# Kernel tuning notes

Measured on AMD Instinct MI355X. Metric: run time of the kernel, lower is better.

Reference implementation:

```python
import jax, jax.numpy as jnp
import numpy as np

A = -0.75  # torch bicubic coefficient
SCALES = [1.0, 0.9, 0.8, 0.7, 0.6]  # level=5
SOFTMAX_SCALE = 10.0
RES_SCALE = 1.0
ESCAPE_NAN = 1e-4


def _cubic_w(d):
    d = jnp.abs(d)
    return jnp.where(d <= 1.0, ((A + 2.0) * d - (A + 3.0)) * d * d + 1.0,
                     jnp.where(d < 2.0, ((A * d - 5.0 * A) * d + 8.0 * A) * d - 4.0 * A, 0.0))


def _resize_axis(x, out_size, axis):
    # bicubic, align_corners=True, 4-tap cubic conv with border clamp (matches torch)
    in_size = x.shape[axis]
    src = jnp.arange(out_size, dtype=jnp.float32) * (float(in_size - 1) / float(out_size - 1))
    i0 = jnp.floor(src).astype(jnp.int32)
    frac = src - i0.astype(jnp.float32)
    idx = jnp.clip(jnp.stack([i0 - 1, i0, i0 + 1, i0 + 2], 0), 0, in_size - 1)  # [4,out]
    w = jnp.stack([_cubic_w(frac + 1.0), _cubic_w(frac), _cubic_w(1.0 - frac), _cubic_w(2.0 - frac)], 0)  # [4,out]
    xm = jnp.moveaxis(x, axis, 0)
    g = xm[idx]  # [4,out,...]
    out = jnp.einsum('ko...,ko->o...', g, w)
    return jnp.moveaxis(out, 0, axis)


def bicubic_resize(x, oh, ow):
    return _resize_axis(_resize_axis(x, oh, 2), ow, 3)


def prelu(x, a):
    return jnp.where(x >= 0, x, a * x)


def conv1x1(x, W, b):
    # x [B,C,H,W], W [O,C], b [O]
    return jnp.einsum('oc,bchw->bohw', W, x) + b[None, :, None, None]


def extract_patches(x):
    # x [B,C,H,W] -> [B, H*W, C, 3, 3], 'same' padding, stride 1 (torch unfold order C,kh,kw)
    B, C, H, Wd = x.shape
    xp = jnp.pad(x, ((0, 0), (0, 0), (1, 1), (1, 1)))
    sl = [xp[:, :, dy:dy + H, dx:dx + Wd] for dy in range(3) for dx in range(3)]
    p = jnp.stack(sl, 0).reshape(3, 3, B, C, H, Wd)
    p = jnp.transpose(p, (2, 4, 5, 3, 0, 1))  # [B,H,W,C,3,3]
    return p.reshape(B, H * Wd, C, 3, 3)


def setup_inputs() -> dict:
    key = jax.random.key(0)
    ks = jax.random.split(key, 8)
    B, C, H, Wd = 2, 64, 64, 64
    Cm = 32
    return {
        'input': jax.random.normal(ks[0], (B, C, H, Wd), jnp.float32),
        'input_ref': jax.random.normal(ks[1], (B, C, H, Wd), jnp.float32),
        'Wb': jax.random.normal(ks[2], (Cm, C), jnp.float32) * 0.1,
        'bb': jax.random.normal(ks[3], (Cm,), jnp.float32) * 0.01,
        'Wm': jax.random.normal(ks[4], (Cm, C), jnp.float32) * 0.1,
        'bm': jax.random.normal(ks[5], (Cm,), jnp.float32) * 0.01,
        'Wa': jax.random.normal(ks[6], (C, C), jnp.float32) * 0.1,
        'ba': jax.random.normal(ks[7], (C,), jnp.float32) * 0.01,
        'a_prelu': jnp.full((1,), 0.25, jnp.float32),
    }


def reference(input, input_ref, Wb, bb, Wm, bm, Wa, ba, a_prelu):
    B, C, H, Wd = input.shape
    a = a_prelu[0]
    match_base = prelu(conv1x1(input, Wb, bb), a)  # [B,Cm,H,W]

    w_list, rw_list = [], []
    for s in SCALES:
        ref = input_ref if s == 1.0 else bicubic_resize(input_ref, int(H * s), int(Wd * s))
        base = prelu(conv1x1(ref, Wa, ba), a)   # conv_assembly
        rw_list.append(extract_patches(base))   # [B,Li,C,3,3]
        m = prelu(conv1x1(ref, Wm, bm), a)      # conv_match
        w_list.append(extract_patches(m))       # [B,Li,Cm,3,3]
    w = jnp.concatenate(w_list, axis=1)    # [B,L,Cm,3,3]
    rw = jnp.concatenate(rw_list, axis=1)  # [B,L,C,3,3]

    dn = ('NCHW', 'OIHW', 'NCHW')

    def per_sample(xi, wi, rwi):
        # xi [Cm,H,W]; wi [L,Cm,3,3]; rwi [L,C,3,3]
        nrm = jnp.maximum(jnp.sqrt(jnp.sum(wi * wi, axis=(1, 2, 3), keepdims=True)), ESCAPE_NAN)
        wn = wi / nrm
        scores = jax.lax.conv_general_dilated(xi[None], wn, (1, 1), [(1, 1), (1, 1)], dimension_numbers=dn)[0]  # [L,H,W]
        yi = jax.nn.softmax(scores * SOFTMAX_SCALE, axis=0)
        # conv_transpose2d(yi, rwi, stride=1, padding=1) == conv2d with flipped, transposed kernel, pad 1
        k = jnp.transpose(rwi, (1, 0, 2, 3))[:, :, ::-1, ::-1]  # [C,L,3,3]
        out = jax.lax.conv_general_dilated(yi[None], k, (1, 1), [(1, 1), (1, 1)], dimension_numbers=dn)[0] / 4.0
        return out  # [C,H,W]

    y = jax.vmap(per_sample)(match_base, w, rw)
    return y + input * RES_SCALE
```

## Files before the change

### kernel.cpp

```cpp
#include <hip/hip_runtime.h>
#include <stdint.h>


typedef __attribute__((ext_vector_type(8))) short bf16x8;
typedef __attribute__((ext_vector_type(4))) float f32x4;
typedef unsigned short ushort_t;

#define L_TOT  13326
#define NCHT   417
#define NPIX   4096
#define BCHUNK_E 9216
#define RCHUNK_E 18432
#define LOG2E10 14.4269504f
#define CT 256

__device__ __forceinline__ float cubw(float d) {
  d = fabsf(d);
  if (d <= 1.f) return (1.25f * d - 2.25f) * d * d + 1.f;
  if (d < 2.f)  return ((-0.75f * d + 3.75f) * d - 6.f) * d + 3.f;
  return 0.f;
}

__device__ __forceinline__ void decode_l(int l, int& S, int& off) {
  if (l < 4096)       { S = 64; off = 0; }
  else if (l < 7345)  { S = 57; off = 4096; }
  else if (l < 9946)  { S = 51; off = 7345; }
  else if (l < 11882) { S = 44; off = 9946; }
  else                { S = 38; off = 11882; }
}

__device__ __forceinline__ ushort_t f2bf(float f) {
  union { float f; uint32_t u; } v; v.f = f;
  uint32_t r = (v.u + 0x7fffu + ((v.u >> 16) & 1u)) >> 16;
  return (ushort_t)r;
}

__device__ __forceinline__ float preluf(float x, float a) { return x >= 0.f ? x : a * x; }

__device__ __forceinline__ void gll16(const ushort_t* g, ushort_t* l) {
  __builtin_amdgcn_global_load_lds(
      (const __attribute__((address_space(1))) unsigned int*)g,
      (__attribute__((address_space(3))) unsigned int*)l, 16, 0, 0);
}

__global__ void k_convref(const float* __restrict__ inref,
                          const float* __restrict__ Wm, const float* __restrict__ bm,
                          const float* __restrict__ Wa, const float* __restrict__ ba,
                          const float* __restrict__ ap,
                          float* __restrict__ mref, float* __restrict__ aref) {
  __shared__ float T[64][CT];
  __shared__ float Wy[CT][5], Wx[CT][5];
  __shared__ int   IY[CT], IX[CT];
  int blk = blockIdx.x;
  int oh = blk & 1; int lt = (blk >> 1) % 53; int b = blk / 106;
  int l0 = lt * CT;
  int tid = threadIdx.x;
  float a = ap[0];
  {
    int gl = l0 + tid;
    if (gl < L_TOT) {
      int S, off; decode_l(gl, S, off);
      int li = gl - off; int ly = li / S, lx = li % S;
      if (S == 64) {
        IY[tid] = -1; IX[tid] = ly * 64 + lx;
      } else {
        float sc = (float)(63.0 / (double)(S - 1));
        float sy = (float)ly * sc, sx = (float)lx * sc;
        int iy = (int)floorf(sy), ix = (int)floorf(sx);
        float fy = sy - (float)iy, fx = sx - (float)ix;
        IY[tid] = iy; IX[tid] = ix;
        Wy[tid][0] = cubw(fy + 1.f); Wy[tid][1] = cubw(fy);
        Wy[tid][2] = cubw(1.f - fy); Wy[tid][3] = cubw(2.f - fy);
        Wx[tid][0] = cubw(fx + 1.f); Wx[tid][1] = cubw(fx);
        Wx[tid][2] = cubw(1.f - fx); Wx[tid][3] = cubw(2.f - fx);
      }
    }
  }
  __syncthreads();
  for (int i = tid; i < 64 * CT; i += 256) {
    int c = i >> 8; int l2 = i & 255;
    int gl = l0 + l2;
    float val = 0.f;
    if (gl < L_TOT) {
      const float* img = inref + (size_t)(b * 64 + c) * 4096;
      int iy = IY[l2];
      if (iy == -1) {
        val = img[IX[l2]];
      } else {
        int ix = IX[l2];
        #pragma unroll
        for (int t = 0; t < 4; ++t) {
          int ty = iy - 1 + t; ty = ty < 0 ? 0 : (ty > 63 ? 63 : ty);
          float rv = 0.f;
          #pragma unroll
          for (int u = 0; u < 4; ++u) {
            int tx = ix - 1 + u; tx = tx < 0 ? 0 : (tx > 63 ? 63 : tx);
            rv += Wx[l2][u] * img[ty * 64 + tx];
          }
          val += Wy[l2][t] * rv;
        }
      }
    }
    T[c][l2] = val;
  }
  __syncthreads();
  int gl = l0 + tid;
  if (gl >= L_TOT) return;
  for (int oc = oh * 48; oc < oh * 48 + 48; ++oc) {
    const float* Wrow; float s;
    if (oc < 32) { Wrow = Wm + oc * 64; s = bm[oc]; }
    else         { Wrow = Wa + (oc - 32) * 64; s = ba[oc - 32]; }
    #pragma unroll 8
    for (int c = 0; c < 64; ++c) s += Wrow[c] * T[c][tid];
    s = preluf(s, a);
    if (oc < 32) mref[(size_t)(b * 32 + oc) * L_TOT + gl] = s;
    else         aref[(size_t)(b * 64 + oc - 32) * L_TOT + gl] = s;
  }
}

__global__ void k_mb(const float* __restrict__ input, const float* __restrict__ Wb,
                     const float* __restrict__ bb, const float* __restrict__ ap,
                     float* __restrict__ mbb, int n) {
  int idx = blockIdx.x * 256 + threadIdx.x;
  if (idx >= n) return;
  int p = idx % NPIX; int cm = (idx / NPIX) % 32; int b = idx / (32 * NPIX);
  float a = ap[0];
  float acc = bb[cm];
  for (int c = 0; c < 64; ++c) acc += Wb[cm * 64 + c] * input[(size_t)(b * 64 + c) * NPIX + p];
  mbb[(size_t)(b * 32 + cm) * NPIX + p] = preluf(acc, a);
}

__global__ void k_stage1(const float* __restrict__ mref, const float* __restrict__ mbb,
                         float* __restrict__ ssq, float* __restrict__ ssqA, int n) {
  int idx = blockIdx.x * 256 + threadIdx.x;
  if (idx >= n) return;
  if (idx < 2 * L_TOT) {
    int l = idx % L_TOT; int b = idx / L_TOT;
    float s = 0.f;
    for (int c = 0; c < 32; ++c) { float v = mref[(size_t)(b * 32 + c) * L_TOT + l]; s += v * v; }
    ssq[idx] = s;
  } else {
    int j = idx - 2 * L_TOT;
    int p = j % NPIX; int b = j / NPIX;
    float s = 0.f;
    for (int c = 0; c < 32; ++c) { float v = mbb[(size_t)(b * 32 + c) * NPIX + p]; s += v * v; }
    ssqA[j] = s;
  }
}

__global__ void k_stage2(const float* __restrict__ ssq, const float* __restrict__ ssqA,
                         float* __restrict__ invn, float* __restrict__ Mlog, int n) {
  int idx = blockIdx.x * 256 + threadIdx.x;
  if (idx >= n) return;
  if (idx < 2 * L_TOT) {
    int l = idx % L_TOT; int b = idx / L_TOT;
    int S, off; decode_l(l, S, off);
    int li = l - off; int ly = li / S, lx = li % S;
    float acc = 0.f;
    for (int dy = -1; dy <= 1; ++dy) {
      int ny = ly + dy; if (ny < 0 || ny >= S) continue;
      for (int dx = -1; dx <= 1; ++dx) {
        int nx = lx + dx; if (nx < 0 || nx >= S) continue;
        acc += ssq[(size_t)b * L_TOT + off + ny * S + nx];
      }
    }
    float nrm = sqrtf(acc); nrm = fmaxf(nrm, 1e-4f);
    invn[idx] = 1.f / nrm;
  } else {
    int j = idx - 2 * L_TOT;
    int p = j % NPIX; int b = j / NPIX;
    int y = p / 64, x = p % 64;
    float acc = 0.f;
    for (int dy = -1; dy <= 1; ++dy) {
      int ny = y + dy; if (ny < 0 || ny >= 64) continue;
      for (int dx = -1; dx <= 1; ++dx) {
        int nx = x + dx; if (nx < 0 || nx >= 64) continue;
        acc += ssqA[(size_t)b * NPIX + ny * 64 + nx];
      }
    }
    float qn = sqrtf(acc);
    float m = fmaxf(0.7f * qn, qn - 7.f);
    Mlog[j] = LOG2E10 * m;
  }
}

#define N_BS (2 * NCHT * 1152)
#define N_AIM (2 * NPIX * 36)
#define N_RS (2 * NCHT * 576 * 4)
__global__ void k_pack(const float* __restrict__ mref, const float* __restrict__ invn,
                       const float* __restrict__ mbb, const float* __restrict__ aref,
                       ushort_t* __restrict__ Bs, ushort_t* __restrict__ Am,
                       ushort_t* __restrict__ Rs, int n) {
  int idx = blockIdx.x * 256 + threadIdx.x;
  if (idx >= n) return;
  ushort_t v[8];
  if (idx < N_BS) {
    int segp = idx % 36; int col = (idx / 36) % 32;
    int ch = (idx / 1152) % NCHT; int b = idx / (1152 * NCHT);
    int segl = (segp & ~3) | ((segp & 3) ^ ((col >> 1) & 3));
    int l = ch * 32 + col;
    if (l < L_TOT) {
      int S, off; decode_l(l, S, off);
      int li = l - off; int ly = li / S, lx = li % S;
      float iv = invn[(size_t)b * L_TOT + l];
      #pragma unroll
      for (int e = 0; e < 8; ++e) {
        int k = segl * 8 + e;
        int c = k / 9; int r = k % 9; int dy = r / 3 - 1, dx = r % 3 - 1;
        int ny = ly + dy, nx = lx + dx;
        float val = 0.f;
        if (ny >= 0 && ny < S && nx >= 0 && nx < S)
          val = mref[(size_t)(b * 32 + c) * L_TOT + off + ny * S + nx] * iv;
        v[e] = f2bf(val);
      }
    } else {
      #pragma unroll
      for (int e = 0; e < 8; ++e) v[e] = 0;
    }
    *(uint4*)(Bs + ((size_t)(b * NCHT + ch) * BCHUNK_E + col * 288 + segp * 8)) = *(const uint4*)v;
  } else if (idx < N_BS + N_AIM) {
    int j = idx - N_BS;
    int k8 = j % 36; int p = (j / 36) % NPIX; int b = j / (36 * NPIX);
    int y = p / 64, x = p % 64;
    #pragma unroll
    for (int e = 0; e < 8; ++e) {
      int k = k8 * 8 + e;
      int c = k / 9; int r = k % 9; int dy = r / 3 - 1, dx = r % 3 - 1;
      int ny = y + dy, nx = x + dx;
      float val = 0.f;
      if (ny >= 0 && ny < 64 && nx >= 0 && nx < 64)
        val = mbb[(size_t)(b * 32 + c) * NPIX + ny * 64 + nx];
      v[e] = f2bf(val);
    }
    *(uint4*)(Am + ((size_t)(b * NPIX + p) * 288 + k8 * 8)) = *(const uint4*)v;
  } else {
    int j = idx - N_BS - N_AIM;
    int phys = j & 3; int q = j >> 2;
    int col = q % 576; q /= 576;
    int ch = q % NCHT; int b = q / NCHT;
    int c = col / 9; int r = col % 9; int dy = r / 3 - 1, dx = r % 3 - 1;
    int seg = phys ^ ((col >> 1) & 3);
    int lbase = ch * 32 + seg * 8;
    #pragma unroll
    for (int e = 0; e < 8; ++e) {
      int l = lbase + e;
      float val = 0.f;
      if (l < L_TOT) {
        int S, off; decode_l(l, S, off);
        int li = l - off; int ly = li / S, lx = li % S;
        int ny = ly + dy, nx = lx + dx;
        if (ny >= 0 && ny < S && nx >= 0 && nx < S)
          val = aref[(size_t)(b * 64 + c) * L_TOT + off + ny * S + nx];
      }
      v[e] = f2bf(val);
    }
    *(uint4*)(Rs + ((size_t)(b * NCHT + ch) * RCHUNK_E + col * 32 + phys * 8)) = *(const uint4*)v;
  }
}

__global__ __launch_bounds__(512, 2) void k_attn64(const ushort_t* __restrict__ Am,
                                                   const ushort_t* __restrict__ Bs,
                                                   const ushort_t* __restrict__ Rs,
                                                   const float* __restrict__ Mlog,
                                                   float* __restrict__ Og,
                                                   float* __restrict__ Ol) {
  __shared__ ushort_t Rl[3][RCHUNK_E];
  __shared__ ushort_t Bl[2][BCHUNK_E];
  __shared__ ushort_t Pl[2][2048];
  int tid = threadIdx.x;
  int xcd = blockIdx.x & 7; int slot = blockIdx.x >> 3;
  int group = xcd >> 1;
  int spl = group & 1; int b = group >> 1;
  int tile = slot * 2 + (xcd & 1);
  int p0 = tile * 64;
  int wave = tid >> 6, lane = tid & 63, quad = lane >> 4, ln = lane & 15;
  int rbS = wave & 3, cbh = wave >> 2;
  int g = wave & 3, zrh = wave >> 2;
  int c0 = spl ? 209 : 0, c1 = spl ? NCHT : 209;

  bf16x8 af[9];
  {
    const ushort_t* arow = Am + (size_t)(b * NPIX + p0 + rbS * 16 + ln) * 288;
    #pragma unroll
    for (int kk = 0; kk < 9; ++kk) af[kk] = *(const bf16x8*)(arow + kk * 32 + quad * 8);
  }
  float mlg[4];
  #pragma unroll
  for (int r = 0; r < 4; ++r)
    mlg[r] = Mlog[(size_t)b * NPIX + p0 + rbS * 16 + quad * 4 + r];

  f32x4 acc[2][9];
  #pragma unroll
  for (int h = 0; h < 2; ++h)
    #pragma unroll
    for (int t = 0; t < 9; ++t) { acc[h][t][0] = acc[h][t][1] = acc[h][t][2] = acc[h][t][3] = 0.f; }
  float psum[4] = {0.f, 0.f, 0.f, 0.f};

  const ushort_t* RsB = Rs + (size_t)b * NCHT * RCHUNK_E + lane * 8;
  const ushort_t* BsB = Bs + (size_t)b * NCHT * BCHUNK_E + lane * 8;

  {
    const ushort_t* sB0 = BsB + (size_t)c0 * BCHUNK_E;
    ushort_t* dB0 = Bl[c0 & 1];
    #pragma unroll
    for (int u = wave; u < 18; u += 8) gll16(sB0 + u * 512, dB0 + u * 512);
    const ushort_t* sB1 = BsB + (size_t)(c0 + 1) * BCHUNK_E;
    ushort_t* dB1 = Bl[(c0 + 1) & 1];
    #pragma unroll
    for (int u = wave; u < 18; u += 8) gll16(sB1 + u * 512, dB1 + u * 512);
    const ushort_t* sR = RsB + (size_t)c0 * RCHUNK_E;
    ushort_t* dR = Rl[c0 % 3];
    #pragma unroll
    for (int u = wave; u < 36; u += 8) gll16(sR + u * 512, dR + u * 512);
  }
  __syncthreads();

  int col32 = cbh * 16 + ln;
  int bswz = (col32 >> 1) & 3;
  int rpar = c0 % 3;
  for (int ch = c0; ch < c1; ++ch) {
    int par = ch & 1;
    int rnext = rpar == 2 ? 0 : rpar + 1;
    f32x4 sa, sb;
    sa[0] = sa[1] = sa[2] = sa[3] = 0.f;
    sb[0] = sb[1] = sb[2] = sb[3] = 0.f;
    #pragma unroll
    for (int kk = 0; kk < 9; ++kk) {
      int segp = kk * 4 + (quad ^ bswz);
      bf16x8 bf = *(const bf16x8*)&Bl[par][col32 * 288 + segp * 8];
      if (kk == 4 || kk == 5 || kk == 6 || kk == 7)
        sb = __builtin_amdgcn_mfma_f32_16x16x32_bf16(af[kk], bf, sb, 0, 0, 0);
      else
        sa = __builtin_amdgcn_mfma_f32_16x16x32_bf16(af[kk], bf, sa, 0, 0, 0);
    }
    int colw = ch * 32 + col32;
    bool valid = colw < L_TOT;
    #pragma unroll
    for (int r = 0; r < 4; ++r) {
      float sv = sa[r] + sb[r];
      float pv = valid ? exp2f(fmaf(sv, LOG2E10, -mlg[r])) : 0.f;
      int row = rbS * 16 + quad * 4 + r;
      int seg = cbh * 2 + (ln >> 3);
      int swz = seg ^ ((row >> 1) & 3);
      Pl[par][row * 32 + swz * 8 + (ln & 7)] = f2bf(pv);
      psum[r] += pv;
    }
    __syncthreads();
    if (ch + 2 < c1) {
      const ushort_t* sB = BsB + (size_t)(ch + 2) * BCHUNK_E;
      ushort_t* dB = Bl[par];
      #pragma unroll
      for (int u = wave; u < 18; u += 8) gll16(sB + u * 512, dB + u * 512);
    }
    if (ch + 1 < c1) {
      const ushort_t* sR = RsB + (size_t)(ch + 1) * RCHUNK_E;
      ushort_t* dR = Rl[rnext];
      #pragma unroll
      for (int u = wave; u < 36; u += 8) gll16(sR + u * 512, dR + u * 512);
    }
    bf16x8 pf0, pf1;
    {
      int sw = quad ^ ((ln >> 1) & 3);
      pf0 = *(const bf16x8*)&Pl[par][(zrh * 32 + ln) * 32 + sw * 8];
      pf1 = *(const bf16x8*)&Pl[par][(zrh * 32 + 16 + ln) * 32 + sw * 8];
    }
    #pragma unroll
    for (int t = 0; t < 9; ++t) {
      int col = g * 144 + t * 16 + ln;
      int swz = quad ^ ((col >> 1) & 3);
      bf16x8 rf = *(const bf16x8*)&Rl[rpar][col * 32 + swz * 8];
      acc[0][t] = __builtin_amdgcn_mfma_f32_16x16x32_bf16(pf0, rf, acc[0][t], 0, 0, 0);
      acc[1][t] = __builtin_amdgcn_mfma_f32_16x16x32_bf16(pf1, rf, acc[1][t], 0, 0, 0);
    }
    rpar = rnext;
  }

  #pragma unroll
  for (int m = 1; m <= 8; m <<= 1)
    #pragma unroll
    for (int r = 0; r < 4; ++r) psum[r] += __shfl_xor(psum[r], m);
  int sb2 = spl * 2 + b;
  if (ln == 0) {
    #pragma unroll
    for (int r = 0; r < 4; ++r) {
      int row = p0 + rbS * 16 + quad * 4 + r;
      Ol[(size_t)(sb2 * 2 + cbh) * NPIX + row] = psum[r];
    }
  }
  #pragma unroll
  for (int h = 0; h < 2; ++h)
    #pragma unroll
    for (int t = 0; t < 9; ++t) {
      int colg = g * 144 + t * 16 + ln;
      #pragma unroll
      for (int r = 0; r < 4; ++r) {
        int row = p0 + zrh * 32 + h * 16 + quad * 4 + r;
        Og[((size_t)sb2 * NPIX + row) * 576 + colg] = acc[h][t][r];
      }
    }
}

__global__ __launch_bounds__(512, 2) void k_attn128(const ushort_t* __restrict__ Am,
                                                    const ushort_t* __restrict__ Bs,
                                                    const ushort_t* __restrict__ Rs,
                                                    const float* __restrict__ Mlog,
                                                    float* __restrict__ Og,
                                                    float* __restrict__ Ol) {
  __shared__ ushort_t Rl[2][RCHUNK_E];
  __shared__ ushort_t Bl[2][BCHUNK_E];
  __shared__ ushort_t Pl[2][4096];
  int tid = threadIdx.x;
  int xcd = blockIdx.x & 7; int slot = blockIdx.x >> 3;
  int spl = xcd >> 1; int b = xcd & 1;
  int p0 = slot * 128;
  int wave = tid >> 6, lane = tid & 63, quad = lane >> 4, ln = lane & 15;
  int rb = wave;
  int g = wave & 3, zrh = wave >> 2;
  int c0 = (spl * NCHT) >> 2;
  int c1 = ((spl + 1) * NCHT) >> 2;

  bf16x8 af[9];
  {
    const ushort_t* arow = Am + (size_t)(b * NPIX + p0 + rb * 16 + ln) * 288;
    #pragma unroll
    for (int kk = 0; kk < 9; ++kk) af[kk] = *(const bf16x8*)(arow + kk * 32 + quad * 8);
  }
  float mlg[4], psum[4];
  #pragma unroll
  for (int r = 0; r < 4; ++r) {
    mlg[r] = Mlog[(size_t)b * NPIX + p0 + rb * 16 + quad * 4 + r];
    psum[r] = 0.f;
  }
  f32x4 acc[4][9];
  #pragma unroll
  for (int j = 0; j < 4; ++j)
    #pragma unroll
    for (int t = 0; t < 9; ++t) { acc[j][t][0] = acc[j][t][1] = acc[j][t][2] = acc[j][t][3] = 0.f; }

  const ushort_t* RsB = Rs + (size_t)b * NCHT * RCHUNK_E + lane * 8;
  const ushort_t* BsB = Bs + (size_t)b * NCHT * BCHUNK_E + lane * 8;

  auto stageB = [&](int chunk, int sl) {
    const ushort_t* s = BsB + (size_t)chunk * BCHUNK_E;
    ushort_t* d = Bl[sl];
    #pragma unroll
    for (int u = wave; u < 18; u += 8) gll16(s + u * 512, d + u * 512);
  };
  auto stageR = [&](int chunk, int sl) {
    const ushort_t* s = RsB + (size_t)chunk * RCHUNK_E;
    ushort_t* d = Rl[sl];
    #pragma unroll
    for (int u = wave; u < 36; u += 8) gll16(s + u * 512, d + u * 512);
  };

  int bswz = (ln >> 1) & 3;
  int psw = quad ^ ((ln >> 1) & 3);

  stageB(c0, 0);
  stageB(c0 + 1, 1);
  stageR(c0, 0);
  __syncthreads();

  for (int ch = c0; ch < c1; ++ch) {
    int par = ch & 1;
    f32x4 sA0, sB0, sA1, sB1;
    sA0[0]=sA0[1]=sA0[2]=sA0[3]=0.f; sB0[0]=sB0[1]=sB0[2]=sB0[3]=0.f;
    sA1[0]=sA1[1]=sA1[2]=sA1[3]=0.f; sB1[0]=sB1[1]=sB1[2]=sB1[3]=0.f;
    #pragma unroll
    for (int kk = 0; kk < 9; ++kk) {
      int segp = kk * 4 + (quad ^ bswz);
      bf16x8 bf0 = *(const bf16x8*)&Bl[par][(ln) * 288 + segp * 8];
      bf16x8 bf1 = *(const bf16x8*)&Bl[par][(16 + ln) * 288 + segp * 8];
      if (kk >= 4 && kk <= 7) {
        sB0 = __builtin_amdgcn_mfma_f32_16x16x32_bf16(af[kk], bf0, sB0, 0, 0, 0);
        sB1 = __builtin_amdgcn_mfma_f32_16x16x32_bf16(af[kk], bf1, sB1, 0, 0, 0);
      } else {
        sA0 = __builtin_amdgcn_mfma_f32_16x16x32_bf16(af[kk], bf0, sA0, 0, 0, 0);
        sA1 = __builtin_amdgcn_mfma_f32_16x16x32_bf16(af[kk], bf1, sA1, 0, 0, 0);
      }
    }
    bool valid0 = ch * 32 + ln < L_TOT;
    bool valid1 = ch * 32 + 16 + ln < L_TOT;
    #pragma unroll
    for (int r = 0; r < 4; ++r) {
      int row = rb * 16 + quad * 4 + r;
      int rsw = (row >> 1) & 3;
      float sv0 = sA0[r] + sB0[r];
      float pv0 = valid0 ? exp2f(fmaf(sv0, LOG2E10, -mlg[r])) : 0.f;
      int seg0 = 0 * 2 + (ln >> 3);
      Pl[par][row * 32 + (seg0 ^ rsw) * 8 + (ln & 7)] = f2bf(pv0);
      float sv1 = sA1[r] + sB1[r];
      float pv1 = valid1 ? exp2f(fmaf(sv1, LOG2E10, -mlg[r])) : 0.f;
      int seg1 = 1 * 2 + (ln >> 3);
      Pl[par][row * 32 + (seg1 ^ rsw) * 8 + (ln & 7)] = f2bf(pv1);
      psum[r] += pv0 + pv1;
    }
    __syncthreads();
    if (ch + 2 < c1) stageB(ch + 2, par);
    if (ch + 1 < c1) stageR(ch + 1, par ^ 1);
    bf16x8 pf[4];
    #pragma unroll
    for (int j = 0; j < 4; ++j)
      pf[j] = *(const bf16x8*)&Pl[par][(zrh * 64 + j * 16 + ln) * 32 + psw * 8];
    #pragma unroll
    for (int t = 0; t < 9; ++t) {
      int col = g * 144 + t * 16 + ln;
      int swz = quad ^ ((col >> 1) & 3);
      bf16x8 rf = *(const bf16x8*)&Rl[par][col * 32 + swz * 8];
      #pragma unroll
      for (int j = 0; j < 4; ++j)
        acc[j][t] = __builtin_amdgcn_mfma_f32_16x16x32_bf16(pf[j], rf, acc[j][t], 0, 0, 0);
    }
  }

  #pragma unroll
  for (int m = 1; m <= 8; m <<= 1)
    #pragma unroll
    for (int r = 0; r < 4; ++r) psum[r] += __shfl_xor(psum[r], m);
  int sb2 = spl * 2 + b;
  if (ln == 0) {
    #pragma unroll
    for (int r = 0; r < 4; ++r) {
      int row = p0 + rb * 16 + quad * 4 + r;
      Ol[(size_t)sb2 * NPIX + row] = psum[r];
    }
  }
  #pragma unroll
  for (int j = 0; j < 4; ++j)
    #pragma unroll
    for (int t = 0; t < 9; ++t) {
      int colg = g * 144 + t * 16 + ln;
      #pragma unroll
      for (int r = 0; r < 4; ++r) {
        int row = p0 + zrh * 64 + j * 16 + quad * 4 + r;
        Og[((size_t)sb2 * NPIX + row) * 576 + colg] = acc[j][t][r];
      }
    }
}

template <int IS128>
__global__ void k_inv(const float* __restrict__ Ol, float* __restrict__ inv, int n) {
  int idx = blockIdx.x * 256 + threadIdx.x;
  if (idx >= n) return;
  int b = idx / NPIX; int p = idx % NPIX;
  float s = 0.f;
  if (IS128) {
    #pragma unroll
    for (int spl = 0; spl < 4; ++spl)
      s += Ol[(size_t)(spl * 2 + b) * NPIX + p];
  } else {
    #pragma unroll
    for (int spl = 0; spl < 2; ++spl)
      #pragma unroll
      for (int cbh = 0; cbh < 2; ++cbh)
        s += Ol[(size_t)(((spl * 2 + b) * 2) + cbh) * NPIX + p];
  }
  inv[idx] = 1.f / s;
}

template <int NSL>
__global__ __launch_bounds__(256) void k_final(const float* __restrict__ Og,
                                               const float* __restrict__ inv,
                                               const float* __restrict__ input,
                                               float* __restrict__ out) {
  __shared__ float Srow[34][577];
  int blk = blockIdx.x;
  int xh = blk & 1; int y = (blk >> 1) & 63; int b = blk >> 7;
  int tid = threadIdx.x;
  const size_t S1 = (size_t)2 * NPIX * 576;
  int x32 = tid & 31, c0 = (tid >> 5) * 8;
  int qx0 = xh * 32 - 1;
  float acc[8];
  #pragma unroll
  for (int i = 0; i < 8; ++i) acc[i] = 0.f;

  for (int j = 0; j < 3; ++j) {
    int qy = y + 1 - j;
    if (qy < 0 || qy >= 64) continue;
    for (int u = tid; u < 34 * 144; u += 256) {
      int k = u / 144; int f4 = u - k * 144;
      int qx = qx0 + k;
      float vx = 0.f, vy = 0.f, vz = 0.f, vw = 0.f;
      if (qx >= 0 && qx < 64) {
        int p = qy * 64 + qx;
        size_t e = ((size_t)b * NPIX + p) * 576 + f4 * 4;
        float iv = inv[b * NPIX + p];
        #pragma unroll
        for (int s = 0; s < NSL; ++s) {
          const float4 t4 = *(const float4*)(Og + e + (size_t)s * S1);
          vx += t4.x; vy += t4.y; vz += t4.z; vw += t4.w;
        }
        vx *= iv; vy *= iv; vz *= iv; vw *= iv;
      }
      float* d = &Srow[k][f4 * 4];
      d[0] = vx; d[1] = vy; d[2] = vz; d[3] = vw;
    }
    __syncthreads();
    #pragma unroll
    for (int i2 = 0; i2 < 3; ++i2) {
      int k = x32 + 2 - i2;
      #pragma unroll
      for (int cc = 0; cc < 8; ++cc)
        acc[cc] += Srow[k][(c0 + cc) * 9 + j * 3 + i2];
    }
    __syncthreads();
  }

  int x = xh * 32 + x32;
  #pragma unroll
  for (int cc = 0; cc < 8; ++cc) {
    int c = c0 + cc;
    int o = ((b * 64 + c) * 64 + y) * 64 + x;
    out[o] = 0.25f * acc[cc] + input[o];
  }
}

extern "C" void kernel_launch(void* const* d_in, const int* in_sizes, int n_in,
                              void* d_out, int out_size, void* d_ws, size_t ws_size,
                              hipStream_t stream) {
  (void)in_sizes; (void)n_in; (void)out_size;
  const float* input = (const float*)d_in[0];
  const float* inref = (const float*)d_in[1];
  const float* Wb = (const float*)d_in[2];
  const float* bb = (const float*)d_in[3];
  const float* Wm = (const float*)d_in[4];
  const float* bm = (const float*)d_in[5];
  const float* Wa = (const float*)d_in[6];
  const float* ba = (const float*)d_in[7];
  const float* ap = (const float*)d_in[8];
  float* out = (float*)d_out;

  char* ws = (char*)d_ws;
  size_t off = 0;
  auto alloc = [&](size_t bytes) -> char* {
    char* p = ws + off; off = (off + bytes + 255) & ~(size_t)255; return p;
  };
  ushort_t* Am   = (ushort_t*)alloc((size_t)2 * NPIX * 288 * 2);
  ushort_t* Bs   = (ushort_t*)alloc((size_t)2 * NCHT * BCHUNK_E * 2);
  ushort_t* Rs   = (ushort_t*)alloc((size_t)2 * NCHT * RCHUNK_E * 2);
  float*    Ol   = (float*)alloc((size_t)16 * NPIX * 4);
  float*    inv  = (float*)alloc((size_t)2 * NPIX * 4);
  float*    Mlog = (float*)alloc((size_t)2 * NPIX * 4);
  float*    ssqA = (float*)alloc((size_t)2 * NPIX * 4);
  size_t og64  = (size_t)4 * NPIX * 576 * 4;
  size_t og128 = og64 * 2;
  bool use128 = (off + og128 + 512) <= ws_size;
  char* big = alloc(use128 ? og128 : og64);
  float* Og = (float*)big;
  size_t eoff = 0;
  auto ealloc = [&](size_t bytes) -> char* {
    char* p = big + eoff; eoff = (eoff + bytes + 255) & ~(size_t)255; return p;
  };
  float* mref = (float*)ealloc((size_t)2 * 32 * L_TOT * 4);
  float* aref = (float*)ealloc((size_t)2 * 64 * L_TOT * 4);
  float* mbb  = (float*)ealloc((size_t)2 * 32 * NPIX * 4);
  float* ssq  = (float*)ealloc((size_t)2 * L_TOT * 4);
  float* invn = (float*)ealloc((size_t)2 * L_TOT * 4);

  k_convref<<<212, 256, 0, stream>>>(inref, Wm, bm, Wa, ba, ap, mref, aref);
  int n3 = 2 * 32 * NPIX;
  k_mb<<<(n3 + 255) / 256, 256, 0, stream>>>(input, Wb, bb, ap, mbb, n3);
  int ns = 2 * L_TOT + 2 * NPIX;
  k_stage1<<<(ns + 255) / 256, 256, 0, stream>>>(mref, mbb, ssq, ssqA, ns);
  k_stage2<<<(ns + 255) / 256, 256, 0, stream>>>(ssq, ssqA, invn, Mlog, ns);
  int np = N_BS + N_AIM + N_RS;
  k_pack<<<(np + 255) / 256, 256, 0, stream>>>(mref, invn, mbb, aref, Bs, Am, Rs, np);

  if (use128) {
    k_attn128<<<256, 512, 0, stream>>>(Am, Bs, Rs, Mlog, Og, Ol);
    k_inv<1><<<(2 * NPIX + 255) / 256, 256, 0, stream>>>(Ol, inv, 2 * NPIX);
    k_final<4><<<256, 256, 0, stream>>>(Og, inv, input, out);
  } else {
    k_attn64<<<256, 512, 0, stream>>>(Am, Bs, Rs, Mlog, Og, Ol);
    k_inv<0><<<(2 * NPIX + 255) / 256, 256, 0, stream>>>(Ol, inv, 2 * NPIX);
    k_final<2><<<256, 256, 0, stream>>>(Og, inv, input, out);
  }
}
```

Measured before the change: 439.0 us.

## Stage pack inputs in LDS, pre-reduce split outputs, split conv accumulators

The pack kernel is rebuilt as one block per chunk or pixel tile. Each block stages the needed window of mref, aref, invn or mbb in shared memory and then builds the Bs, Rs and Am bf16 tiles, so repeated uncached global gathers become LDS reads. On the 128 path, a new k_redog kernel adds the four split partial outputs together so k_final reads a single slice. The 1x1 conv loops in k_convref and k_mb now use four independent accumulators to shorten the dependency chain. The cost is extra launches, a large shared-memory footprint per pack block, and a small change in floating-point summation order.

New measurement: 479.6 us. 9.2% more time.

```diff
diff --git a/kernel.cpp b/kernel.cpp
--- a/kernel.cpp
+++ b/kernel.cpp
@@ -13,6 +13,8 @@
 #define RCHUNK_E 18432
 #define LOG2E10 14.4269504f
 #define CT 256
+#define PKW 169
+#define PKWA 393
 
 __device__ __forceinline__ float cubw(float d) {
   d = fabsf(d);
@@ -107,11 +109,18 @@
   int gl = l0 + tid;
   if (gl >= L_TOT) return;
   for (int oc = oh * 48; oc < oh * 48 + 48; ++oc) {
-    const float* Wrow; float s;
-    if (oc < 32) { Wrow = Wm + oc * 64; s = bm[oc]; }
-    else         { Wrow = Wa + (oc - 32) * 64; s = ba[oc - 32]; }
-    #pragma unroll 8
-    for (int c = 0; c < 64; ++c) s += Wrow[c] * T[c][tid];
+    const float* Wrow; float bias;
+    if (oc < 32) { Wrow = Wm + oc * 64; bias = bm[oc]; }
+    else         { Wrow = Wa + (oc - 32) * 64; bias = ba[oc - 32]; }
+    float s0 = 0.f, s1 = 0.f, s2 = 0.f, s3 = 0.f;
+    #pragma unroll 4
+    for (int c = 0; c < 64; c += 4) {
+      s0 += Wrow[c]     * T[c][tid];
+      s1 += Wrow[c + 1] * T[c + 1][tid];
+      s2 += Wrow[c + 2] * T[c + 2][tid];
+      s3 += Wrow[c + 3] * T[c + 3][tid];
+    }
+    float s = bias + ((s0 + s1) + (s2 + s3));
     s = preluf(s, a);
     if (oc < 32) mref[(size_t)(b * 32 + oc) * L_TOT + gl] = s;
     else         aref[(size_t)(b * 64 + oc - 32) * L_TOT + gl] = s;
@@ -125,8 +134,16 @@
   if (idx >= n) return;
   int p = idx % NPIX; int cm = (idx / NPIX) % 32; int b = idx / (32 * NPIX);
   float a = ap[0];
-  float acc = bb[cm];
-  for (int c = 0; c < 64; ++c) acc += Wb[cm * 64 + c] * input[(size_t)(b * 64 + c) * NPIX + p];
+  const float* ip = input + (size_t)b * 64 * NPIX + p;
+  const float* wr = Wb + cm * 64;
+  float a0 = 0.f, a1 = 0.f, a2 = 0.f, a3 = 0.f;
+  for (int c = 0; c < 64; c += 4) {
+    a0 += wr[c]     * ip[(size_t)c * NPIX];
+    a1 += wr[c + 1] * ip[(size_t)(c + 1) * NPIX];
+    a2 += wr[c + 2] * ip[(size_t)(c + 2) * NPIX];
+    a3 += wr[c + 3] * ip[(size_t)(c + 3) * NPIX];
+  }
+  float acc = bb[cm] + ((a0 + a1) + (a2 + a3));
   mbb[(size_t)(b * 32 + cm) * NPIX + p] = preluf(acc, a);
 }
 
@@ -184,77 +201,107 @@
   }
 }
 
-#define N_BS (2 * NCHT * 1152)
-#define N_AIM (2 * NPIX * 36)
-#define N_RS (2 * NCHT * 576 * 4)
-__global__ void k_pack(const float* __restrict__ mref, const float* __restrict__ invn,
-                       const float* __restrict__ mbb, const float* __restrict__ aref,
-                       ushort_t* __restrict__ Bs, ushort_t* __restrict__ Am,
-                       ushort_t* __restrict__ Rs, int n) {
-  int idx = blockIdx.x * 256 + threadIdx.x;
-  if (idx >= n) return;
-  ushort_t v[8];
-  if (idx < N_BS) {
-    int segp = idx % 36; int col = (idx / 36) % 32;
-    int ch = (idx / 1152) % NCHT; int b = idx / (1152 * NCHT);
-    int segl = (segp & ~3) | ((segp & 3) ^ ((col >> 1) & 3));
-    int l = ch * 32 + col;
-    if (l < L_TOT) {
-      int S, off; decode_l(l, S, off);
-      int li = l - off; int ly = li / S, lx = li % S;
-      float iv = invn[(size_t)b * L_TOT + l];
-      #pragma unroll
-      for (int e = 0; e < 8; ++e) {
-        int k = segl * 8 + e;
-        int c = k / 9; int r = k % 9; int dy = r / 3 - 1, dx = r % 3 - 1;
-        int ny = ly + dy, nx = lx + dx;
-        float val = 0.f;
-        if (ny >= 0 && ny < S && nx >= 0 && nx < S)
-          val = mref[(size_t)(b * 32 + c) * L_TOT + off + ny * S + nx] * iv;
-        v[e] = f2bf(val);
-      }
-    } else {
-      #pragma unroll
-      for (int e = 0; e < 8; ++e) v[e] = 0;
-    }
-    *(uint4*)(Bs + ((size_t)(b * NCHT + ch) * BCHUNK_E + col * 288 + segp * 8)) = *(const uint4*)v;
-  } else if (idx < N_BS + N_AIM) {
-    int j = idx - N_BS;
-    int k8 = j % 36; int p = (j / 36) % NPIX; int b = j / (36 * NPIX);
-    int y = p / 64, x = p % 64;
-    #pragma unroll
-    for (int e = 0; e < 8; ++e) {
-      int k = k8 * 8 + e;
-      int c = k / 9; int r = k % 9; int dy = r / 3 - 1, dx = r % 3 - 1;
-      int ny = y + dy, nx = x + dx;
-      float val = 0.f;
-      if (ny >= 0 && ny < 64 && nx >= 0 && nx < 64)
-        val = mbb[(size_t)(b * 32 + c) * NPIX + ny * 64 + nx];
-      v[e] = f2bf(val);
-    }
-    *(uint4*)(Am + ((size_t)(b * NPIX + p) * 288 + k8 * 8)) = *(const uint4*)v;
-  } else {
-    int j = idx - N_BS - N_AIM;
-    int phys = j & 3; int q = j >> 2;
-    int col = q % 576; q /= 576;
-    int ch = q % NCHT; int b = q / NCHT;
-    int c = col / 9; int r = col % 9; int dy = r / 3 - 1, dx = r % 3 - 1;
-    int seg = phys ^ ((col >> 1) & 3);
-    int lbase = ch * 32 + seg * 8;
-    #pragma unroll
-    for (int e = 0; e < 8; ++e) {
-      int l = lbase + e;
-      float val = 0.f;
+__global__ __launch_bounds__(256) void k_pack2(const float* __restrict__ mref,
+                                               const float* __restrict__ invn,
+                                               const float* __restrict__ mbb,
+                                               const float* __restrict__ aref,
+                                               ushort_t* __restrict__ Bs,
+                                               ushort_t* __restrict__ Am,
+                                               ushort_t* __restrict__ Rs) {
+  __shared__ float LS[97 * PKW];
+  int blk = blockIdx.x; int tid = threadIdx.x;
+  if (blk < 2 * NCHT) {
+    int b = blk / NCHT, ch = blk % NCHT;
+    int lo = ch * 32 - 66; if (lo < 0) lo = 0;
+    int hi = ch * 32 + 98; if (hi > L_TOT) hi = L_TOT;
+    int W = hi - lo;
+    float* Lm = LS;
+    float* La = LS + 32 * PKW;
+    float* Li = LS + 96 * PKW;
+    for (int u = tid; u < 32 * W; u += 256) {
+      int c = u / W, i = u - c * W;
+      Lm[c * PKW + i] = mref[(size_t)(b * 32 + c) * L_TOT + lo + i];
+    }
+    for (int u = tid; u < 64 * W; u += 256) {
+      int c = u / W, i = u - c * W;
+      La[c * PKW + i] = aref[(size_t)(b * 64 + c) * L_TOT + lo + i];
+    }
+    for (int i = tid; i < W; i += 256) Li[i] = invn[(size_t)b * L_TOT + lo + i];
+    __syncthreads();
+    for (int u = tid; u < 1152; u += 256) {
+      int segp = u % 36, col = u / 36;
+      int segl = (segp & ~3) | ((segp & 3) ^ ((col >> 1) & 3));
+      int l = ch * 32 + col;
+      ushort_t v[8];
       if (l < L_TOT) {
         int S, off; decode_l(l, S, off);
         int li = l - off; int ly = li / S, lx = li % S;
-        int ny = ly + dy, nx = lx + dx;
-        if (ny >= 0 && ny < S && nx >= 0 && nx < S)
-          val = aref[(size_t)(b * 64 + c) * L_TOT + off + ny * S + nx];
-      }
-      v[e] = f2bf(val);
-    }
-    *(uint4*)(Rs + ((size_t)(b * NCHT + ch) * RCHUNK_E + col * 32 + phys * 8)) = *(const uint4*)v;
+        float iv = Li[l - lo];
+        #pragma unroll
+        for (int e = 0; e < 8; ++e) {
+          int k = segl * 8 + e;
+          int c = k / 9; int r = k % 9; int dy = r / 3 - 1, dx = r % 3 - 1;
+          int ny = ly + dy, nx = lx + dx;
+          float val = 0.f;
+          if (ny >= 0 && ny < S && nx >= 0 && nx < S)
+            val = Lm[c * PKW + (off + ny * S + nx - lo)] * iv;
+          v[e] = f2bf(val);
+        }
+      } else {
+        #pragma unroll
+        for (int e = 0; e < 8; ++e) v[e] = 0;
+      }
+      *(uint4*)(Bs + ((size_t)(b * NCHT + ch) * BCHUNK_E + col * 288 + segp * 8)) = *(const uint4*)v;
+    }
+    for (int u = tid; u < 2304; u += 256) {
+      int phys = u & 3; int col = u >> 2;
+      int c = col / 9; int r = col % 9; int dy = r / 3 - 1, dx = r % 3 - 1;
+      int seg = phys ^ ((col >> 1) & 3);
+      int lbase = ch * 32 + seg * 8;
+      ushort_t v[8];
+      #pragma unroll
+      for (int e = 0; e < 8; ++e) {
+        int l = lbase + e;
+        float val = 0.f;
+        if (l < L_TOT) {
+          int S, off; decode_l(l, S, off);
+          int li = l - off; int ly = li / S, lx = li % S;
+          int ny = ly + dy, nx = lx + dx;
+          if (ny >= 0 && ny < S && nx >= 0 && nx < S)
+            val = La[c * PKW + (off + ny * S + nx - lo)];
+        }
+        v[e] = f2bf(val);
+      }
+      *(uint4*)(Rs + ((size_t)(b * NCHT + ch) * RCHUNK_E + col * 32 + phys * 8)) = *(const uint4*)v;
+    }
+  } else {
+    int a2 = blk - 2 * NCHT;
+    int b = a2 >> 4; int p0 = (a2 & 15) * 256;
+    int lo = p0 - 65; if (lo < 0) lo = 0;
+    int hi = p0 + 256 + 65; if (hi > NPIX) hi = NPIX;
+    int W = hi - lo;
+    float* Lp = LS;
+    for (int u = tid; u < 32 * W; u += 256) {
+      int c = u / W, i = u - c * W;
+      Lp[c * PKWA + i] = mbb[(size_t)(b * 32 + c) * NPIX + lo + i];
+    }
+    __syncthreads();
+    for (int u = tid; u < 9216; u += 256) {
+      int k8 = u % 36; int p = p0 + u / 36;
+      int y = p / 64, x = p % 64;
+      ushort_t v[8];
+      #pragma unroll
+      for (int e = 0; e < 8; ++e) {
+        int k = k8 * 8 + e;
+        int c = k / 9; int r = k % 9; int dy = r / 3 - 1, dx = r % 3 - 1;
+        int ny = y + dy, nx = x + dx;
+        float val = 0.f;
+        if (ny >= 0 && ny < 64 && nx >= 0 && nx < 64)
+          val = Lp[c * PKWA + (p + dy * 64 + dx - lo)];
+        v[e] = f2bf(val);
+      }
+      *(uint4*)(Am + ((size_t)(b * NPIX + p) * 288 + k8 * 8)) = *(const uint4*)v;
+    }
   }
 }
 
@@ -556,6 +603,21 @@
         s += Ol[(size_t)(((spl * 2 + b) * 2) + cbh) * NPIX + p];
   }
   inv[idx] = 1.f / s;
+}
+
+__global__ void k_redog(float* __restrict__ Og) {
+  const size_t S1 = (size_t)2 * NPIX * 576;
+  size_t i = ((size_t)blockIdx.x * 256 + threadIdx.x) * 4;
+  if (i >= S1) return;
+  float4 a = *(const float4*)(Og + i);
+  float4 b1 = *(const float4*)(Og + i + S1);
+  float4 c = *(const float4*)(Og + i + 2 * S1);
+  float4 d = *(const float4*)(Og + i + 3 * S1);
+  a.x += b1.x + c.x + d.x;
+  a.y += b1.y + c.y + d.y;
+  a.z += b1.z + c.z + d.z;
+  a.w += b1.w + c.w + d.w;
+  *(float4*)(Og + i) = a;
 }
 
 template <int NSL>
@@ -663,13 +725,14 @@
   int ns = 2 * L_TOT + 2 * NPIX;
   k_stage1<<<(ns + 255) / 256, 256, 0, stream>>>(mref, mbb, ssq, ssqA, ns);
   k_stage2<<<(ns + 255) / 256, 256, 0, stream>>>(ssq, ssqA, invn, Mlog, ns);
-  int np = N_BS + N_AIM + N_RS;
-  k_pack<<<(np + 255) / 256, 256, 0, stream>>>(mref, invn, mbb, aref, Bs, Am, Rs, np);
+  k_pack2<<<2 * NCHT + 32, 256, 0, stream>>>(mref, invn, mbb, aref, Bs, Am, Rs);
 
   if (use128) {
     k_attn128<<<256, 512, 0, stream>>>(Am, Bs, Rs, Mlog, Og, Ol);
+    int nred = (2 * NPIX * 576) / 4;
+    k_redog<<<(nred + 255) / 256, 256, 0, stream>>>(Og);
     k_inv<1><<<(2 * NPIX + 255) / 256, 256, 0, stream>>>(Ol, inv, 2 * NPIX);
-    k_final<4><<<256, 256, 0, stream>>>(Og, inv, input, out);
+    k_final<1><<<256, 256, 0, stream>>>(Og, inv, input, out);
   } else {
     k_attn64<<<256, 512, 0, stream>>>(Am, Bs, Rs, Mlog, Og, Ol);
     k_inv<0><<<(2 * NPIX + 255) / 256, 256, 0, stream>>>(Ol, inv, 2 * NPIX);
```
